# Performance work log

Measured on AMD Instinct MI355X. Metric: run time of the kernel, lower is better.

Reference implementation:

```python
import jax, jax.numpy as jnp
import numpy as np

B, T, E, D = 64, 512, 1024, 1024  # batch, enc timesteps, enc hidden, dec hidden


def setup_inputs() -> dict:
    key = jax.random.key(0)
    ks = jax.random.split(key, 9)
    s = lambda fan_in: 1.0 / np.sqrt(fan_in)
    return {
        "hidden": jax.random.normal(ks[0], (B, D), jnp.float32),
        "decoder_out": jax.random.normal(ks[1], (B, D), jnp.float32),
        "encoder_states": jax.random.normal(ks[2], (T, B, E), jnp.float32),
        # attn: Linear(D+E -> 2E)
        "Wa": jax.random.uniform(ks[3], (2 * E, D + E), jnp.float32, -s(D + E), s(D + E)),
        "ba": jax.random.uniform(ks[4], (2 * E,), jnp.float32, -s(D + E), s(D + E)),
        # attn2: Linear(2E -> 1)
        "w2": jax.random.uniform(ks[5], (1, 2 * E), jnp.float32, -s(2 * E), s(2 * E)),
        "b2": jax.random.uniform(ks[6], (1,), jnp.float32, -s(2 * E), s(2 * E)),
        # attn_combine: Linear(D+E -> D)
        "Wc": jax.random.uniform(ks[7], (D, D + E), jnp.float32, -s(D + E), s(D + E)),
        "bc": jax.random.uniform(ks[8], (D,), jnp.float32, -s(D + E), s(D + E)),
    }


def reference(hidden, decoder_out, encoder_states, Wa, ba, w2, b2, Wc, bc):
    d = hidden.shape[1]
    # attn(cat(hidden, enc_t)) = hidden @ Wa[:, :D].T + enc_t @ Wa[:, D:].T + ba
    h_proj = hidden @ Wa[:, :d].T + ba                      # [B, 2E]
    e_proj = jnp.einsum('tbe,fe->tbf', encoder_states, Wa[:, d:])  # [T, B, 2E]
    act = jnp.tanh(h_proj[None, :, :] + e_proj)             # [T, B, 2E]
    scores = jnp.einsum('tbf,f->bt', act, w2[0]) + b2[0]    # [B, T]
    weights = jax.nn.softmax(scores, axis=-1)               # softmax over timesteps
    # weighted sum of encoder states: [B, E]
    applied = jnp.einsum('bt,tbe->be', weights, encoder_states)
    combined = jnp.concatenate([decoder_out, applied], axis=1)  # [B, D+E]
    out = jnp.tanh(combined @ Wc.T + bc)                    # [B, D]
    return out, applied
```

## Files before the change

### kernel.cpp

```cpp
#include <hip/hip_runtime.h>
#include <hip/hip_bf16.h>

#define BB 64
#define TT 512
#define EE 1024
#define DD 1024
#define BK 64

typedef __attribute__((ext_vector_type(8))) short s16x8;
typedef __attribute__((ext_vector_type(4))) float f32x4;

__device__ __forceinline__ float bf2f(unsigned short u) {
    unsigned int x = ((unsigned int)u) << 16;
    return __builtin_bit_cast(float, x);
}
__device__ __forceinline__ unsigned short f2bf(float f) {
    unsigned int u = __builtin_bit_cast(unsigned int, f);
    u += 0x7FFF + ((u >> 16) & 1);
    return (unsigned short)(u >> 16);
}
__device__ __forceinline__ float tanh_fast(float x) {
    x = fminf(fmaxf(x, -15.f), 15.f);
    float e = __expf(2.f * x);
    return (e - 1.f) / (e + 1.f);
}

__device__ __forceinline__ int tile_slot(int row, int g) {
    return (row >> 4) * 128 + (g >> 2) * 64 + (g & 3) * 16 + (row & 15);
}

__global__ __launch_bounds__(256) void conv_encS_kernel(
    const float* __restrict__ enc, unsigned short* __restrict__ encS)
{
    __shared__ short tileL[1024 * 8];
    const int tm  = blockIdx.x;
    const int tk  = blockIdx.y;
    const int tid = threadIdx.x;

#pragma unroll
    for (int it = 0; it < 4; ++it) {
        int cidx = it * 256 + tid;
        int row  = cidx >> 3;
        int g    = cidx & 7;
        const float* src = enc + (size_t)(tm * 128 + row) * 1024 + tk * 64 + g * 8;
        float4 v0 = ((const float4*)src)[0];
        float4 v1 = ((const float4*)src)[1];
        short c[8];
        c[0] = (short)f2bf(v0.x); c[1] = (short)f2bf(v0.y);
        c[2] = (short)f2bf(v0.z); c[3] = (short)f2bf(v0.w);
        c[4] = (short)f2bf(v1.x); c[5] = (short)f2bf(v1.y);
        c[6] = (short)f2bf(v1.z); c[7] = (short)f2bf(v1.w);
        *(s16x8*)&tileL[tile_slot(row, g) * 8] = *(s16x8*)c;
    }
    __syncthreads();
    unsigned short* dst = encS + ((size_t)tm * 16 + tk) * 8192;
#pragma unroll
    for (int it = 0; it < 4; ++it) {
        int s = it * 256 + tid;
        *(s16x8*)&dst[s * 8] = *(const s16x8*)&tileL[s * 8];
    }
}

__global__ __launch_bounds__(256) void conv_waS_kernel(
    const float* __restrict__ Wa, unsigned short* __restrict__ WaS)
{
    __shared__ short tileL[1024 * 8];
    const int tn  = blockIdx.x;
    const int tk  = blockIdx.y;
    const int tid = threadIdx.x;

#pragma unroll
    for (int it = 0; it < 4; ++it) {
        int cidx = it * 256 + tid;
        int row  = cidx >> 3;
        int g    = cidx & 7;
        const float* src = Wa + (size_t)(tn * 128 + row) * 2048 + 1024 + tk * 64 + g * 8;
        float4 v0 = ((const float4*)src)[0];
        float4 v1 = ((const float4*)src)[1];
        short c[8];
        c[0] = (short)f2bf(v0.x); c[1] = (short)f2bf(v0.y);
        c[2] = (short)f2bf(v0.z); c[3] = (short)f2bf(v0.w);
        c[4] = (short)f2bf(v1.x); c[5] = (short)f2bf(v1.y);
        c[6] = (short)f2bf(v1.z); c[7] = (short)f2bf(v1.w);
        *(s16x8*)&tileL[tile_slot(row, g) * 8] = *(s16x8*)c;
    }
    __syncthreads();
    unsigned short* dst = WaS + ((size_t)tn * 16 + tk) * 8192;
#pragma unroll
    for (int it = 0; it < 4; ++it) {
        int s = it * 256 + tid;
        *(s16x8*)&dst[s * 8] = *(const s16x8*)&tileL[s * 8];
    }
}

__global__ __launch_bounds__(256) void hproj_kernel(
    const float* __restrict__ hidden,
    const float* __restrict__ Wa,
    const float* __restrict__ ba,
    float* __restrict__ hp)
{
    __shared__ float sW[8 * 1024];
    const int tid  = threadIdx.x;
    const int lane = tid & 63;
    const int wave = tid >> 6;
    const int f0   = blockIdx.x * 8;

#pragma unroll
    for (int i = 0; i < 8; ++i) {
        int idx = i * 256 + tid;
        int fi  = idx >> 8;
        int c4  = idx & 255;
        ((float4*)sW)[idx] = *(const float4*)(Wa + (size_t)(f0 + fi) * 2048 + c4 * 4);
    }
    __syncthreads();

    for (int bi = 0; bi < 16; ++bi) {
        int b = wave * 16 + bi;
        float h[16];
#pragma unroll
        for (int j = 0; j < 16; ++j) h[j] = hidden[b * 1024 + lane + 64 * j];
#pragma unroll
        for (int fi = 0; fi < 8; ++fi) {
            float s = 0.f;
#pragma unroll
            for (int j = 0; j < 16; ++j) s += h[j] * sW[fi * 1024 + lane + 64 * j];
#pragma unroll
            for (int m = 32; m; m >>= 1) s += __shfl_xor(s, m);
            if (lane == 0) hp[(f0 + fi) * 64 + b] = s + ba[f0 + fi];
        }
    }
}

__global__ __launch_bounds__(256) void gemm_scores(
    const unsigned short* __restrict__ encS,
    const unsigned short* __restrict__ WaS,
    const float* __restrict__ hp,
    const float* __restrict__ w2,
    float* __restrict__ scores)
{
    __shared__ short sA[2][128 * BK];
    __shared__ short sB[2][128 * BK];
    __shared__ float rowAcc[128];

    const int tid  = threadIdx.x;
    const int bid  = blockIdx.x;
    const int w    = (bid & 7) * 512 + (bid >> 3);
    const int bm   = w >> 4;
    const int bn   = w & 15;
    const int lane = tid & 63;
    const int wave = tid >> 6;
    const int wm   = wave >> 1;
    const int wn   = wave & 1;
    const int c    = lane & 15;
    const int quad = lane >> 4;

    f32x4 acc[4][4];
#pragma unroll
    for (int mi = 0; mi < 4; ++mi)
#pragma unroll
        for (int ni = 0; ni < 4; ++ni)
#pragma unroll
            for (int r = 0; r < 4; ++r) acc[mi][ni][r] = 0.f;

    const unsigned short* atBase = encS + (size_t)bm * 16 * 8192;
    const unsigned short* btBase = WaS  + (size_t)bn * 16 * 8192;

    auto STAGE = [&](int kt, int buf) {
        const unsigned short* at = atBase + (size_t)kt * 8192;
        const unsigned short* bt = btBase + (size_t)kt * 8192;
#pragma unroll
        for (int i = 0; i < 4; ++i) {
            int s = i * 256 + tid;
            __builtin_amdgcn_global_load_lds(
                (const __attribute__((address_space(1))) void*)(at + s * 8),
                (__attribute__((address_space(3))) void*)&sA[buf][s * 8], 16, 0, 0);
            __builtin_amdgcn_global_load_lds(
                (const __attribute__((address_space(1))) void*)(bt + s * 8),
                (__attribute__((address_space(3))) void*)&sB[buf][s * 8], 16, 0, 0);
        }
    };

    STAGE(0, 0);
    __syncthreads();

    for (int kt = 0; kt < 16; ++kt) {
        const int cur = kt & 1;
        if (kt < 15) STAGE(kt + 1, cur ^ 1);

#pragma unroll
        for (int kk = 0; kk < 2; ++kk) {
            s16x8 aF[4], bF[4];
#pragma unroll
            for (int mi = 0; mi < 4; ++mi)
                aF[mi] = *(const s16x8*)&sA[cur][((wm * 4 + mi) * 128 + kk * 64 + lane) * 8];
#pragma unroll
            for (int ni = 0; ni < 4; ++ni)
                bF[ni] = *(const s16x8*)&sB[cur][((wn * 4 + ni) * 128 + kk * 64 + lane) * 8];

            __builtin_amdgcn_s_setprio(1);
#pragma unroll
            for (int mi = 0; mi < 4; ++mi)
#pragma unroll
                for (int ni = 0; ni < 4; ++ni)
                    acc[mi][ni] = __builtin_amdgcn_mfma_f32_16x16x32_bf16(
                        aF[mi], bF[ni], acc[mi][ni], 0, 0, 0);
            __builtin_amdgcn_s_setprio(0);
        }
        __syncthreads();
    }

    float w2v[4];
#pragma unroll
    for (int ni = 0; ni < 4; ++ni) w2v[ni] = w2[bn * 128 + wn * 64 + ni * 16 + c];

    if (tid < 128) rowAcc[tid] = 0.f;
    __syncthreads();

#pragma unroll
    for (int mi = 0; mi < 4; ++mi) {
        int lrow0 = wm * 64 + mi * 16 + quad * 4;
        int b0    = (bm * 128 + lrow0) & 63;
        f32x4 hp4[4];
#pragma unroll
        for (int ni = 0; ni < 4; ++ni)
            hp4[ni] = *(const f32x4*)&hp[(bn * 128 + wn * 64 + ni * 16 + c) * 64 + b0];
#pragma unroll
        for (int r = 0; r < 4; ++r) {
            float s = 0.f;
#pragma unroll
            for (int ni = 0; ni < 4; ++ni)
                s += tanh_fast(acc[mi][ni][r] + hp4[ni][r]) * w2v[ni];
            s += __shfl_xor(s, 1);
            s += __shfl_xor(s, 2);
            s += __shfl_xor(s, 4);
            s += __shfl_xor(s, 8);
            if (c == 0) atomicAdd(&rowAcc[lrow0 + r], s);
        }
    }
    __syncthreads();
    if (tid < 128) {
        int grow = bm * 128 + tid;
        int b = grow & 63;
        int t = grow >> 6;
        atomicAdd(&scores[b * TT + t], rowAcc[tid]);
    }
}

__global__ __launch_bounds__(256) void softmax_kernel(float* __restrict__ scores)
{
    __shared__ float wmax[4];
    __shared__ float wsum[4];
    const int b   = blockIdx.x;
    const int tid = threadIdx.x;
    float* row = scores + b * TT;

    float v0 = row[tid], v1 = row[tid + 256];
    float m = fmaxf(v0, v1);
#pragma unroll
    for (int s = 32; s; s >>= 1) m = fmaxf(m, __shfl_xor(m, s));
    if ((tid & 63) == 0) wmax[tid >> 6] = m;
    __syncthreads();
    m = fmaxf(fmaxf(wmax[0], wmax[1]), fmaxf(wmax[2], wmax[3]));

    float e0 = __expf(v0 - m), e1 = __expf(v1 - m);
    float s = e0 + e1;
#pragma unroll
    for (int t = 32; t; t >>= 1) s += __shfl_xor(s, t);
    if ((tid & 63) == 0) wsum[tid >> 6] = s;
    __syncthreads();
    float inv = 1.f / (wsum[0] + wsum[1] + wsum[2] + wsum[3]);
    row[tid]       = e0 * inv;
    row[tid + 256] = e1 * inv;
}

__global__ __launch_bounds__(256) void applied_part_kernel(
    const float* __restrict__ enc,
    const float* __restrict__ w,
    float* __restrict__ part)
{
    __shared__ float red[128 * 8];
    const int tc  = blockIdx.x;
    const int b   = blockIdx.y;
    const int tid = threadIdx.x;
    const int eo  = tid & 127;
    const int th  = tid >> 7;
    const int e0  = eo * 8;

    float a[8];
#pragma unroll
    for (int j = 0; j < 8; ++j) a[j] = 0.f;

    for (int it = 0; it < 16; ++it) {
        int t = tc * 32 + th * 16 + it;
        float wt = w[b * TT + t];
        const float* src = enc + ((size_t)(t * BB + b)) * EE + e0;
        float4 v0 = ((const float4*)src)[0];
        float4 v1 = ((const float4*)src)[1];
        a[0] += wt * v0.x; a[1] += wt * v0.y; a[2] += wt * v0.z; a[3] += wt * v0.w;
        a[4] += wt * v1.x; a[5] += wt * v1.y; a[6] += wt * v1.z; a[7] += wt * v1.w;
    }
    if (th == 1) {
#pragma unroll
        for (int j = 0; j < 8; ++j) red[eo * 8 + j] = a[j];
    }
    __syncthreads();
    if (th == 0) {
        float* dst = part + ((size_t)tc * 64 + b) * 1024 + e0;
#pragma unroll
        for (int j = 0; j < 8; ++j) dst[j] = a[j] + red[eo * 8 + j];
    }
}

__global__ __launch_bounds__(256) void applied_reduce_kernel(
    const float* __restrict__ part, float* __restrict__ out_applied)
{
    int idx = blockIdx.x * 256 + threadIdx.x;
    float s = 0.f;
#pragma unroll
    for (int tc = 0; tc < 16; ++tc) s += part[tc * 65536 + idx];
    out_applied[idx] = s;
}

__global__ __launch_bounds__(256) void combine_kernel(
    const float* __restrict__ dec,
    const float* applied,
    const float* __restrict__ Wc,
    const float* __restrict__ bc,
    float* out0)
{
    const int g    = blockIdx.x * 4 + (threadIdx.x >> 6);
    const int lane = threadIdx.x & 63;
    const int d    = g >> 6;
    const int b    = g & 63;

    const float4* wc4 = (const float4*)Wc + (size_t)d * 512;
    const float4* de4 = (const float4*)dec + (size_t)b * 256;
    const float4* ap4 = (const float4*)applied + (size_t)b * 256;

    float s = 0.f;
#pragma unroll
    for (int j = 0; j < 4; ++j) {
        float4 a = de4[j * 64 + lane];
        float4 wv = wc4[j * 64 + lane];
        s += a.x * wv.x + a.y * wv.y + a.z * wv.z + a.w * wv.w;
    }
#pragma unroll
    for (int j = 0; j < 4; ++j) {
        float4 a = ap4[j * 64 + lane];
        float4 wv = wc4[256 + j * 64 + lane];
        s += a.x * wv.x + a.y * wv.y + a.z * wv.z + a.w * wv.w;
    }
#pragma unroll
    for (int m = 32; m; m >>= 1) s += __shfl_xor(s, m);
    if (lane == 0) out0[b * DD + d] = tanh_fast(s + bc[d]);
}

extern "C" void kernel_launch(void* const* d_in, const int* in_sizes, int n_in,
                              void* d_out, int out_size, void* d_ws, size_t ws_size,
                              hipStream_t stream) {
    const float* hidden = (const float*)d_in[0];
    const float* dec    = (const float*)d_in[1];
    const float* enc    = (const float*)d_in[2];
    const float* Wa     = (const float*)d_in[3];
    const float* ba     = (const float*)d_in[4];
    const float* w2     = (const float*)d_in[5];
    const float* Wc     = (const float*)d_in[7];
    const float* bc     = (const float*)d_in[8];
    float* out = (float*)d_out;

    unsigned short* encS = (unsigned short*)d_ws;
    unsigned short* WaS  = encS + (size_t)33554432;
    float* hp     = (float*)(WaS + (size_t)2097152);
    float* scores = hp + 131072;
    float* part   = scores + 32768;

    hipMemsetAsync(scores, 0, BB * TT * sizeof(float), stream);
    dim3 gc(256, 16);
    conv_encS_kernel<<<gc, 256, 0, stream>>>(enc, encS);
    dim3 gw(16, 16);
    conv_waS_kernel<<<gw, 256, 0, stream>>>(Wa, WaS);
    hproj_kernel<<<256, 256, 0, stream>>>(hidden, Wa, ba, hp);
    gemm_scores<<<4096, 256, 0, stream>>>(encS, WaS, hp, w2, scores);
    softmax_kernel<<<BB, 256, 0, stream>>>(scores);
    dim3 g3(16, 64);
    applied_part_kernel<<<g3, 256, 0, stream>>>(enc, scores, part);
    applied_reduce_kernel<<<256, 256, 0, stream>>>(part, out + BB * DD);
    combine_kernel<<<16384, 256, 0, stream>>>(dec, out + BB * DD, Wc, bc, out);
}
```

Before: 548.2 us.

## Enlarge scores GEMM tile to 256x256 with 8 waves and interleaved prefetch

The scores GEMM moves from 128x128 tiles with 4 waves to 256x256 tiles with 8 waves. Each wave now computes a 128x64 block with 32 accumulators. Loads for the next k-step are split into four pieces issued between the MFMA phases, with explicit vmcnt waits and barriers, so global-to-LDS traffic overlaps with compute. The aim is to raise arithmetic intensity per LDS byte and cut global re-reads of the encoder and weight tiles. In exchange it uses more registers and LDS (128KB), which may limit occupancy, and adds more barriers per k-step.

```diff
diff --git a/kernel.cpp b/kernel.cpp
--- a/kernel.cpp
+++ b/kernel.cpp
@@ -9,6 +9,9 @@
 
 typedef __attribute__((ext_vector_type(8))) short s16x8;
 typedef __attribute__((ext_vector_type(4))) float f32x4;
+
+#define AS1 __attribute__((address_space(1)))
+#define AS3 __attribute__((address_space(3)))
 
 __device__ __forceinline__ float bf2f(unsigned short u) {
     unsigned int x = ((unsigned int)u) << 16;
@@ -131,105 +134,133 @@
     }
 }
 
-__global__ __launch_bounds__(256) void gemm_scores(
+__global__ __launch_bounds__(512, 2) void gemm_scores(
     const unsigned short* __restrict__ encS,
     const unsigned short* __restrict__ WaS,
     const float* __restrict__ hp,
     const float* __restrict__ w2,
     float* __restrict__ scores)
 {
-    __shared__ short sA[2][128 * BK];
-    __shared__ short sB[2][128 * BK];
-    __shared__ float rowAcc[128];
+    __shared__ short sA[2][2][8192];
+    __shared__ short sB[2][2][8192];
+    __shared__ float rowAcc[256];
 
     const int tid  = threadIdx.x;
     const int bid  = blockIdx.x;
-    const int w    = (bid & 7) * 512 + (bid >> 3);
-    const int bm   = w >> 4;
-    const int bn   = w & 15;
+    const int w    = (bid & 7) * 128 + (bid >> 3);
+    const int bm   = w >> 3;
+    const int bn   = w & 7;
     const int lane = tid & 63;
     const int wave = tid >> 6;
-    const int wm   = wave >> 1;
-    const int wn   = wave & 1;
+    const int wm   = wave >> 2;
+    const int wn   = wave & 3;
     const int c    = lane & 15;
     const int quad = lane >> 4;
-
-    f32x4 acc[4][4];
-#pragma unroll
-    for (int mi = 0; mi < 4; ++mi)
-#pragma unroll
-        for (int ni = 0; ni < 4; ++ni)
-#pragma unroll
-            for (int r = 0; r < 4; ++r) acc[mi][ni][r] = 0.f;
-
-    const unsigned short* atBase = encS + (size_t)bm * 16 * 8192;
-    const unsigned short* btBase = WaS  + (size_t)bn * 16 * 8192;
-
-    auto STAGE = [&](int kt, int buf) {
-        const unsigned short* at = atBase + (size_t)kt * 8192;
-        const unsigned short* bt = btBase + (size_t)kt * 8192;
-#pragma unroll
-        for (int i = 0; i < 4; ++i) {
-            int s = i * 256 + tid;
+    const int ntile = wn >> 1;
+    const int nrow0 = (wn & 1) * 4;
+
+    f32x4 acc[8][4];
+#pragma unroll
+    for (int m = 0; m < 8; ++m)
+#pragma unroll
+        for (int n = 0; n < 4; ++n)
+#pragma unroll
+            for (int r = 0; r < 4; ++r) acc[m][n][r] = 0.f;
+
+    const unsigned short* aT = encS + ((size_t)(bm * 2) * 16) * 8192;
+    const unsigned short* bT = WaS  + ((size_t)(bn * 2) * 16) * 8192;
+
+    auto STAGE_PAIR = [&](int kt, int nb, int p) {
+        if (p < 2) {
+            const unsigned short* src = aT + ((size_t)(p * 16 + kt)) * 8192;
             __builtin_amdgcn_global_load_lds(
-                (const __attribute__((address_space(1))) void*)(at + s * 8),
-                (__attribute__((address_space(3))) void*)&sA[buf][s * 8], 16, 0, 0);
+                (const AS1 void*)(src + tid * 8),
+                (AS3 void*)&sA[nb][p][tid * 8], 16, 0, 0);
             __builtin_amdgcn_global_load_lds(
-                (const __attribute__((address_space(1))) void*)(bt + s * 8),
-                (__attribute__((address_space(3))) void*)&sB[buf][s * 8], 16, 0, 0);
+                (const AS1 void*)(src + (512 + tid) * 8),
+                (AS3 void*)&sA[nb][p][(512 + tid) * 8], 16, 0, 0);
+        } else {
+            const int nt = p - 2;
+            const unsigned short* src = bT + ((size_t)(nt * 16 + kt)) * 8192;
+            __builtin_amdgcn_global_load_lds(
+                (const AS1 void*)(src + tid * 8),
+                (AS3 void*)&sB[nb][nt][tid * 8], 16, 0, 0);
+            __builtin_amdgcn_global_load_lds(
+                (const AS1 void*)(src + (512 + tid) * 8),
+                (AS3 void*)&sB[nb][nt][(512 + tid) * 8], 16, 0, 0);
         }
     };
 
-    STAGE(0, 0);
-    __syncthreads();
+#pragma unroll
+    for (int p = 0; p < 4; ++p) STAGE_PAIR(0, 0, p);
 
     for (int kt = 0; kt < 16; ++kt) {
         const int cur = kt & 1;
-        if (kt < 15) STAGE(kt + 1, cur ^ 1);
-
-#pragma unroll
-        for (int kk = 0; kk < 2; ++kk) {
-            s16x8 aF[4], bF[4];
-#pragma unroll
-            for (int mi = 0; mi < 4; ++mi)
-                aF[mi] = *(const s16x8*)&sA[cur][((wm * 4 + mi) * 128 + kk * 64 + lane) * 8];
-#pragma unroll
-            for (int ni = 0; ni < 4; ++ni)
-                bF[ni] = *(const s16x8*)&sB[cur][((wn * 4 + ni) * 128 + kk * 64 + lane) * 8];
-
+        asm volatile("s_waitcnt vmcnt(0)" ::: "memory");
+        __builtin_amdgcn_s_barrier();
+        __builtin_amdgcn_sched_barrier(0);
+        const bool pf = (kt < 15);
+
+        s16x8 bF[2][4];
+#pragma unroll
+        for (int p = 0; p < 4; ++p) {
+            if (p == 0) {
+#pragma unroll
+                for (int n = 0; n < 4; ++n)
+#pragma unroll
+                    for (int kk = 0; kk < 2; ++kk)
+                        bF[kk][n] = *(const s16x8*)
+                            &sB[cur][ntile][((nrow0 + n) * 128 + kk * 64 + lane) * 8];
+            }
+            s16x8 aF[2][2];
+#pragma unroll
+            for (int j = 0; j < 2; ++j)
+#pragma unroll
+                for (int kk = 0; kk < 2; ++kk)
+                    aF[j][kk] = *(const s16x8*)
+                        &sA[cur][wm][((2 * p + j) * 128 + kk * 64 + lane) * 8];
+
+            if (pf) STAGE_PAIR(kt + 1, cur ^ 1, p);
+
+            __builtin_amdgcn_sched_barrier(0);
+            __builtin_amdgcn_s_barrier();
             __builtin_amdgcn_s_setprio(1);
 #pragma unroll
-            for (int mi = 0; mi < 4; ++mi)
-#pragma unroll
-                for (int ni = 0; ni < 4; ++ni)
-                    acc[mi][ni] = __builtin_amdgcn_mfma_f32_16x16x32_bf16(
-                        aF[mi], bF[ni], acc[mi][ni], 0, 0, 0);
+            for (int j = 0; j < 2; ++j)
+#pragma unroll
+                for (int kk = 0; kk < 2; ++kk)
+#pragma unroll
+                    for (int n = 0; n < 4; ++n)
+                        acc[2 * p + j][n] = __builtin_amdgcn_mfma_f32_16x16x32_bf16(
+                            aF[j][kk], bF[kk][n], acc[2 * p + j][n], 0, 0, 0);
             __builtin_amdgcn_s_setprio(0);
+            __builtin_amdgcn_sched_barrier(0);
+            if (p < 3) __builtin_amdgcn_s_barrier();
         }
-        __syncthreads();
-    }
+    }
+
+    __syncthreads();
+    if (tid < 256) rowAcc[tid] = 0.f;
+    __syncthreads();
 
     float w2v[4];
 #pragma unroll
-    for (int ni = 0; ni < 4; ++ni) w2v[ni] = w2[bn * 128 + wn * 64 + ni * 16 + c];
-
-    if (tid < 128) rowAcc[tid] = 0.f;
-    __syncthreads();
-
-#pragma unroll
-    for (int mi = 0; mi < 4; ++mi) {
-        int lrow0 = wm * 64 + mi * 16 + quad * 4;
-        int b0    = (bm * 128 + lrow0) & 63;
+    for (int n = 0; n < 4; ++n) w2v[n] = w2[bn * 256 + wn * 64 + n * 16 + c];
+
+#pragma unroll
+    for (int m = 0; m < 8; ++m) {
+        int lrow0 = wm * 128 + m * 16 + quad * 4;
+        int b0    = lrow0 & 63;
         f32x4 hp4[4];
 #pragma unroll
-        for (int ni = 0; ni < 4; ++ni)
-            hp4[ni] = *(const f32x4*)&hp[(bn * 128 + wn * 64 + ni * 16 + c) * 64 + b0];
+        for (int n = 0; n < 4; ++n)
+            hp4[n] = *(const f32x4*)&hp[(bn * 256 + wn * 64 + n * 16 + c) * 64 + b0];
 #pragma unroll
         for (int r = 0; r < 4; ++r) {
             float s = 0.f;
 #pragma unroll
-            for (int ni = 0; ni < 4; ++ni)
-                s += tanh_fast(acc[mi][ni][r] + hp4[ni][r]) * w2v[ni];
+            for (int n = 0; n < 4; ++n)
+                s += tanh_fast(acc[m][n][r] + hp4[n][r]) * w2v[n];
             s += __shfl_xor(s, 1);
             s += __shfl_xor(s, 2);
             s += __shfl_xor(s, 4);
@@ -238,10 +269,9 @@
         }
     }
     __syncthreads();
-    if (tid < 128) {
-        int grow = bm * 128 + tid;
-        int b = grow & 63;
-        int t = grow >> 6;
+    if (tid < 256) {
+        int b = tid & 63;
+        int t = bm * 4 + (tid >> 6);
         atomicAdd(&scores[b * TT + t], rowAcc[tid]);
     }
 }
@@ -380,7 +410,7 @@
     dim3 gw(16, 16);
     conv_waS_kernel<<<gw, 256, 0, stream>>>(Wa, WaS);
     hproj_kernel<<<256, 256, 0, stream>>>(hidden, Wa, ba, hp);
-    gemm_scores<<<4096, 256, 0, stream>>>(encS, WaS, hp, w2, scores);
+    gemm_scores<<<1024, 512, 0, stream>>>(encS, WaS, hp, w2, scores);
     softmax_kernel<<<BB, 256, 0, stream>>>(scores);
     dim3 g3(16, 64);
     applied_part_kernel<<<g3, 256, 0, stream>>>(enc, scores, part);
```

New measurement: 523.8 us. -4.5%, faster.
